# Performance work log

Measured on AMD Instinct MI355X. Metric: run time of the kernel, lower is better.

Reference implementation:

```python
import jax, jax.numpy as jnp
import numpy as np

TOP_K = 2
NORM_TOPK_PROB = True


def setup_inputs() -> dict:
    key = jax.random.key(0)
    k1, k2, k3, k4 = jax.random.split(key, 4)
    B, S, H = 1, 1024, 2048
    E, I = 16, 768
    hidden_states = jax.random.normal(k1, (B, S, H), dtype=jnp.float32)
    # 0.02 init scale keeps router logits / activations in a realistic range
    gate_w = jax.random.normal(k2, (E, H), dtype=jnp.float32) * 0.02
    w1 = jax.random.normal(k3, (E, 2 * I, H), dtype=jnp.float32) * 0.02  # [gate; up] stacked
    w2 = jax.random.normal(k4, (E, H, I), dtype=jnp.float32) * 0.02
    return {"hidden_states": hidden_states, "gate_w": gate_w, "w1": w1, "w2": w2}


def reference(hidden_states, gate_w, w1, w2):
    B, S, H = hidden_states.shape
    E = gate_w.shape[0]
    I = w2.shape[2]
    x = hidden_states.reshape(-1, H)  # [T, H]

    # Router
    router_logits = x @ gate_w.T  # [T, E]
    probs = jax.nn.softmax(router_logits.astype(jnp.float32), axis=-1)
    topk_w, topk_ids = jax.lax.top_k(probs, TOP_K)  # [T, K]
    if NORM_TOPK_PROB:
        topk_w = topk_w / jnp.sum(topk_w, axis=-1, keepdims=True)
    topk_w = topk_w.astype(x.dtype)

    # combine[t, e] = sum_k topk_w[t, k] * 1[topk_ids[t, k] == e]
    combine = jnp.sum(jax.nn.one_hot(topk_ids, E, dtype=x.dtype) * topk_w[..., None], axis=1)  # [T, E]

    def expert(w1_e, w2_e):
        h = x @ w1_e.T                      # [T, 2I]
        act = jax.nn.silu(h[:, :I]) * h[:, I:]  # fused SiLU-and-mul
        return act @ w2_e.T                 # [T, H]

    y_all = jax.vmap(expert)(w1, w2)        # [E, T, H]
    out = jnp.einsum('te,eth->th', combine, y_all)  # weighted scatter-sum over experts
    return out, router_logits
```

## Files before the change

### kernel.cpp

```cpp
#include <hip/hip_runtime.h>
#include <hip/hip_bf16.h>


#define T_TOK 1024
#define HDIM  2048
#define NEXP  16
#define IDIM  768
#define CAP   192

typedef __attribute__((ext_vector_type(8))) short  short8_t;
typedef __attribute__((ext_vector_type(4))) float  f32x4_t;

static __device__ __forceinline__ unsigned short f2bf(float f) {
  unsigned u = __float_as_uint(f);
  u += 0x7FFFu + ((u >> 16) & 1u);
  return (unsigned short)(u >> 16);
}
static __device__ __forceinline__ short f2bf_t(float f) {
  return (short)(__float_as_uint(f) >> 16);
}
static __device__ __forceinline__ float bf2f(unsigned short h) {
  return __uint_as_float(((unsigned)h) << 16);
}
static __device__ __forceinline__ void cvt_store4(unsigned short* dst, float4 v) {
  ushort4 u;
  u.x = f2bf(v.x); u.y = f2bf(v.y); u.z = f2bf(v.z); u.w = f2bf(v.w);
  *(ushort4*)dst = u;
}
static __device__ __forceinline__ short8_t pack_bf16(float4 lo, float4 hi) {
  short8_t r;
  r[0] = f2bf_t(lo.x); r[1] = f2bf_t(lo.y); r[2] = f2bf_t(lo.z); r[3] = f2bf_t(lo.w);
  r[4] = f2bf_t(hi.x); r[5] = f2bf_t(hi.y); r[6] = f2bf_t(hi.z); r[7] = f2bf_t(hi.w);
  return r;
}
static __device__ __forceinline__ void gl2lds16(const void* g, void* l) {
  __builtin_amdgcn_global_load_lds(
      (const __attribute__((address_space(1))) unsigned int*)g,
      (__attribute__((address_space(3))) unsigned int*)l, 16, 0, 0);
}

__global__ __launch_bounds__(256) void cvt_x(
    const float* __restrict__ x, unsigned short* __restrict__ xb) {
  int i = blockIdx.x * 256 + threadIdx.x;
  float4 v = ((const float4*)x)[i];
  cvt_store4(xb + (size_t)i * 4, v);
}

__global__ __launch_bounds__(256) void moe_router(
    const float* __restrict__ x, const float* __restrict__ gw,
    float* __restrict__ logits_out, int* __restrict__ cnt,
    int* __restrict__ tok, float* __restrict__ wl) {
  const int t = blockIdx.x;
  const int tid = threadIdx.x;
  const int lane = tid & 63, wid = tid >> 6;
  const float4* xv = (const float4*)(x + (size_t)t * HDIM);
  float4 v0 = xv[tid * 2], v1 = xv[tid * 2 + 1];
  float acc[NEXP];
#pragma unroll
  for (int e = 0; e < NEXP; ++e) {
    const float4* gv = (const float4*)(gw + (size_t)e * HDIM);
    float4 g0 = gv[tid * 2], g1 = gv[tid * 2 + 1];
    acc[e] = v0.x * g0.x + v0.y * g0.y + v0.z * g0.z + v0.w * g0.w +
             v1.x * g1.x + v1.y * g1.y + v1.z * g1.z + v1.w * g1.w;
  }
#pragma unroll
  for (int e = 0; e < NEXP; ++e)
#pragma unroll
    for (int off = 32; off; off >>= 1) acc[e] += __shfl_xor(acc[e], off, 64);
  __shared__ float red[4][NEXP];
  if (lane == 0)
#pragma unroll
    for (int e = 0; e < NEXP; ++e) red[wid][e] = acc[e];
  __syncthreads();
  if (tid < NEXP) {
    float s = red[0][tid] + red[1][tid] + red[2][tid] + red[3][tid];
    logits_out[(size_t)t * NEXP + tid] = s;
    red[0][tid] = s;
  }
  __syncthreads();
  if (tid == 0) {
    int e1 = -1, e2 = -1;
    float l1 = -1e30f, l2 = -1e30f;
#pragma unroll
    for (int e = 0; e < NEXP; ++e) {
      float v = red[0][e];
      if (v > l1)      { l2 = l1; e2 = e1; l1 = v; e1 = e; }
      else if (v > l2) { l2 = v;  e2 = e; }
    }
    float wa = 1.f / (1.f + __expf(l2 - l1));
    float wb = 1.f - wa;
    int p1 = atomicAdd(&cnt[e1], 1);
    if (p1 < CAP) { tok[e1 * CAP + p1] = t; wl[e1 * CAP + p1] = wa; }
    int p2 = atomicAdd(&cnt[e2], 1);
    if (p2 < CAP) { tok[e2 * CAP + p2] = t; wl[e2 * CAP + p2] = wb; }
  }
}

__global__ __launch_bounds__(256) void moe_stage_a(
    const unsigned short* __restrict__ xb, const float* __restrict__ w1,
    const int* __restrict__ cnt, const int* __restrict__ tok,
    unsigned short* __restrict__ h_ws) {
  int bx = blockIdx.x;
  const int ks = bx & 1;
  const int mt = (bx >> 1) & 1;
  const int nt = (bx >> 2) % 12;
  const int e  = (bx >> 2) / 12;
  int ne = cnt[e]; if (ne > CAP) ne = CAP;
  if (mt * 128 >= ne) return;

  __shared__ unsigned short As[128 * 32];
  __shared__ float          Bs[128 * 32];
  __shared__ int toksL[128];
  const int tid = threadIdx.x;
  if (tid < 128) {
    int idx = mt * 128 + tid;
    toksL[tid] = tok[e * CAP + (idx < ne ? idx : ne - 1)];
  }
  __syncthreads();

  const int w = tid >> 6, lane = tid & 63;
  const int k0 = ks * 1024;

  const unsigned short* aG[2];
  unsigned short* aL[2];
#pragma unroll
  for (int jj = 0; jj < 2; ++jj) {
    int j = w * 2 + jj;
    int row = 16 * j + (lane >> 2);
    aG[jj] = xb + (size_t)toksL[row] * HDIM + k0 + (lane & 3) * 8;
    aL[jj] = As + j * 512;
  }
  const float* bG[4];
  float* bL[4];
#pragma unroll
  for (int jj = 0; jj < 4; ++jj) {
    int j = w * 4 + jj;
    int nrow = 8 * j + (lane >> 3);
    int d = ((lane & 7) - (lane >> 3)) & 7;
    bG[jj] = w1 + ((size_t)e * (2 * IDIM) + nt * 128 + nrow) * HDIM + k0 + d * 4;
    bL[jj] = Bs + j * 256;
  }

  const int wr = w >> 1, wc = w & 1;
  const int quad = lane >> 4, lr = lane & 15;
  f32x4_t acc[4][4] = {};

  for (int kk = 0; kk < 1024; kk += 32) {
#pragma unroll
    for (int jj = 0; jj < 2; ++jj) gl2lds16(aG[jj] + kk, aL[jj]);
#pragma unroll
    for (int jj = 0; jj < 4; ++jj) gl2lds16(bG[jj] + kk, bL[jj]);
    __syncthreads();

    short8_t a[4], b[4];
#pragma unroll
    for (int mf = 0; mf < 4; ++mf) {
      int row = wr * 64 + mf * 16 + lr;
      a[mf] = *(const short8_t*)&As[row * 32 + quad * 8];
    }
#pragma unroll
    for (int nf = 0; nf < 4; ++nf) {
      int r = wc * 64 + nf * 16 + lr;
      int p0 = (2 * quad + r) & 7, p1 = (2 * quad + 1 + r) & 7;
      float4 f0 = *(const float4*)&Bs[r * 32 + p0 * 4];
      float4 f1 = *(const float4*)&Bs[r * 32 + p1 * 4];
      b[nf] = pack_bf16(f0, f1);
    }
#pragma unroll
    for (int mf = 0; mf < 4; ++mf)
#pragma unroll
      for (int nf = 0; nf < 4; ++nf)
        acc[mf][nf] = __builtin_amdgcn_mfma_f32_16x16x32_bf16(
            a[mf], b[nf], acc[mf][nf], 0, 0, 0);
    __syncthreads();
  }

  unsigned short* hp = h_ws + ((size_t)ks * NEXP + e) * CAP * (2 * IDIM);
#pragma unroll
  for (int mf = 0; mf < 4; ++mf) {
#pragma unroll
    for (int rr = 0; rr < 4; ++rr) {
      int mg = mt * 128 + wr * 64 + mf * 16 + quad * 4 + rr;
      if (mg < CAP) {
#pragma unroll
        for (int nf = 0; nf < 4; ++nf) {
          int ng = nt * 128 + wc * 64 + nf * 16 + lr;
          hp[(size_t)mg * (2 * IDIM) + ng] = f2bf(acc[mf][nf][rr]);
        }
      }
    }
  }
}

__global__ __launch_bounds__(256) void moe_merge(
    const unsigned short* __restrict__ h_ws, unsigned short* __restrict__ act) {
  const size_t part = (size_t)NEXP * CAP * (2 * IDIM);
  int c = blockIdx.x * 256 + threadIdx.x;
  int row = c / (IDIM / 4);
  int c4  = c % (IDIM / 4);
  size_t gb = (size_t)row * (2 * IDIM) + c4 * 4;
  ushort4 g0 = *(const ushort4*)(h_ws + gb);
  ushort4 g1 = *(const ushort4*)(h_ws + part + gb);
  ushort4 u0 = *(const ushort4*)(h_ws + gb + IDIM);
  ushort4 u1 = *(const ushort4*)(h_ws + part + gb + IDIM);
  float g, u; ushort4 o;
  g = bf2f(g0.x) + bf2f(g1.x); u = bf2f(u0.x) + bf2f(u1.x);
  o.x = f2bf(g / (1.f + __expf(-g)) * u);
  g = bf2f(g0.y) + bf2f(g1.y); u = bf2f(u0.y) + bf2f(u1.y);
  o.y = f2bf(g / (1.f + __expf(-g)) * u);
  g = bf2f(g0.z) + bf2f(g1.z); u = bf2f(u0.z) + bf2f(u1.z);
  o.z = f2bf(g / (1.f + __expf(-g)) * u);
  g = bf2f(g0.w) + bf2f(g1.w); u = bf2f(u0.w) + bf2f(u1.w);
  o.w = f2bf(g / (1.f + __expf(-g)) * u);
  *(ushort4*)(act + (size_t)row * IDIM + c4 * 4) = o;
}

__global__ __launch_bounds__(256) void moe_stage_b(
    const unsigned short* __restrict__ act, const float* __restrict__ w2,
    const int* __restrict__ cnt, const int* __restrict__ tok,
    const float* __restrict__ wl, float* __restrict__ out) {
  int bx = blockIdx.x;
  const int ks = bx & 1;
  const int mt = (bx >> 1) & 1;
  const int nt = (bx >> 2) & 15;
  const int e  = bx >> 6;
  int ne = cnt[e]; if (ne > CAP) ne = CAP;
  if (mt * 128 >= ne) return;

  __shared__ unsigned short As[128 * 32];
  __shared__ float          Bs[128 * 32];
  __shared__ int   toksL[128];
  __shared__ float wtsL[128];
  const int tid = threadIdx.x;
  if (tid < 128) {
    int idx = mt * 128 + tid;
    bool v = idx < ne;
    toksL[tid] = tok[e * CAP + (v ? idx : ne - 1)];
    wtsL[tid]  = v ? wl[e * CAP + idx] : 0.f;
  }
  __syncthreads();

  const int w = tid >> 6, lane = tid & 63;
  const int k0 = ks * 384;

  const unsigned short* aG[2];
  unsigned short* aL[2];
#pragma unroll
  for (int jj = 0; jj < 2; ++jj) {
    int j = w * 2 + jj;
    int slot = mt * 128 + 16 * j + (lane >> 2);
    if (slot >= CAP) slot = CAP - 1;
    aG[jj] = act + ((size_t)e * CAP + slot) * IDIM + k0 + (lane & 3) * 8;
    aL[jj] = As + j * 512;
  }
  const float* bG[4];
  float* bL[4];
#pragma unroll
  for (int jj = 0; jj < 4; ++jj) {
    int j = w * 4 + jj;
    int nrow = 8 * j + (lane >> 3);
    int d = ((lane & 7) - (lane >> 3)) & 7;
    bG[jj] = w2 + ((size_t)e * HDIM + nt * 128 + nrow) * IDIM + k0 + d * 4;
    bL[jj] = Bs + j * 256;
  }

  const int wr = w >> 1, wc = w & 1;
  const int quad = lane >> 4, lr = lane & 15;
  f32x4_t acc[4][4] = {};

  for (int kk = 0; kk < 384; kk += 32) {
#pragma unroll
    for (int jj = 0; jj < 2; ++jj) gl2lds16(aG[jj] + kk, aL[jj]);
#pragma unroll
    for (int jj = 0; jj < 4; ++jj) gl2lds16(bG[jj] + kk, bL[jj]);
    __syncthreads();

    short8_t a[4], b[4];
#pragma unroll
    for (int mf = 0; mf < 4; ++mf) {
      int row = wr * 64 + mf * 16 + lr;
      a[mf] = *(const short8_t*)&As[row * 32 + quad * 8];
    }
#pragma unroll
    for (int nf = 0; nf < 4; ++nf) {
      int r = wc * 64 + nf * 16 + lr;
      int p0 = (2 * quad + r) & 7, p1 = (2 * quad + 1 + r) & 7;
      float4 f0 = *(const float4*)&Bs[r * 32 + p0 * 4];
      float4 f1 = *(const float4*)&Bs[r * 32 + p1 * 4];
      b[nf] = pack_bf16(f0, f1);
    }
#pragma unroll
    for (int mf = 0; mf < 4; ++mf)
#pragma unroll
      for (int nf = 0; nf < 4; ++nf)
        acc[mf][nf] = __builtin_amdgcn_mfma_f32_16x16x32_bf16(
            a[mf], b[nf], acc[mf][nf], 0, 0, 0);
    __syncthreads();
  }

#pragma unroll
  for (int mf = 0; mf < 4; ++mf) {
#pragma unroll
    for (int rr = 0; rr < 4; ++rr) {
      int sl = wr * 64 + mf * 16 + quad * 4 + rr;
      if (mt * 128 + sl < ne) {
        float wgt = wtsL[sl];
        int   t   = toksL[sl];
#pragma unroll
        for (int nf = 0; nf < 4; ++nf) {
          int ng = nt * 128 + wc * 64 + nf * 16 + lr;
          atomicAdd(&out[(size_t)t * HDIM + ng], acc[mf][nf][rr] * wgt);
        }
      }
    }
  }
}

extern "C" void kernel_launch(void* const* d_in, const int* in_sizes, int n_in,
                              void* d_out, int out_size, void* d_ws,
                              size_t ws_size, hipStream_t stream) {
  (void)in_sizes; (void)n_in; (void)out_size; (void)ws_size;
  const float* x  = (const float*)d_in[0];
  const float* gw = (const float*)d_in[1];
  const float* w1 = (const float*)d_in[2];
  const float* w2 = (const float*)d_in[3];
  float* out    = (float*)d_out;
  float* logits = out + (size_t)T_TOK * HDIM;

  char* ws = (char*)d_ws;
  int*   cnt = (int*)ws;
  int*   tok = (int*)(ws + 256);
  float* wl  = (float*)(ws + 256 + NEXP * CAP * 4);
  unsigned short* xb  = (unsigned short*)(ws + 24832);
  unsigned short* act = xb;
  unsigned short* h_ws =
      (unsigned short*)(ws + 24832 + (size_t)NEXP * CAP * IDIM * 2);

  hipMemsetAsync(cnt, 0, 256, stream);
  hipMemsetAsync(d_out, 0, (size_t)T_TOK * HDIM * sizeof(float), stream);

  cvt_x      <<<T_TOK * HDIM / 4 / 256, 256, 0, stream>>>(x, xb);
  moe_router <<<T_TOK, 256, 0, stream>>>(x, gw, logits, cnt, tok, wl);
  moe_stage_a<<<NEXP * 12 * 2 * 2, 256, 0, stream>>>(xb, w1, cnt, tok, h_ws);
  moe_merge  <<<NEXP * CAP * IDIM / 4 / 256, 256, 0, stream>>>(h_ws, act);
  moe_stage_b<<<NEXP * 16 * 2 * 2, 256, 0, stream>>>(act, w2, cnt, tok, wl, out);
}
```

Before: 469.0 us.

## Retile expert GEMMs to full-capacity M=192 by N=64 tiles

Both expert GEMM stages change from 128x128 tiles split into two M tiles to a single 192-row tile covering the whole expert capacity, with a 64-wide N tile and each wave owning 48 rows. Each fp32 weight tile is now loaded from global memory once per expert instead of once per M tile. The per-row capacity guard in stage A's store is dropped since 192 equals CAP. The trade-off is that experts with fewer tokens always compute all 192 rows, and the activation tiles are re-read across twice as many N tiles.

```diff
diff --git a/kernel.cpp b/kernel.cpp
--- a/kernel.cpp
+++ b/kernel.cpp
@@ -102,72 +102,66 @@
     unsigned short* __restrict__ h_ws) {
   int bx = blockIdx.x;
   const int ks = bx & 1;
-  const int mt = (bx >> 1) & 1;
-  const int nt = (bx >> 2) % 12;
-  const int e  = (bx >> 2) / 12;
+  const int nt = (bx >> 1) % 24;
+  const int e  = (bx >> 1) / 24;
   int ne = cnt[e]; if (ne > CAP) ne = CAP;
-  if (mt * 128 >= ne) return;
-
-  __shared__ unsigned short As[128 * 32];
-  __shared__ float          Bs[128 * 32];
-  __shared__ int toksL[128];
+
+  __shared__ unsigned short As[192 * 32];
+  __shared__ float          Bs[64 * 32];
+  __shared__ int toksL[192];
   const int tid = threadIdx.x;
-  if (tid < 128) {
-    int idx = mt * 128 + tid;
-    toksL[tid] = tok[e * CAP + (idx < ne ? idx : ne - 1)];
-  }
+  if (tid < 192) toksL[tid] = tok[e * CAP + (tid < ne ? tid : ne - 1)];
   __syncthreads();
 
   const int w = tid >> 6, lane = tid & 63;
   const int k0 = ks * 1024;
 
-  const unsigned short* aG[2];
-  unsigned short* aL[2];
-#pragma unroll
-  for (int jj = 0; jj < 2; ++jj) {
-    int j = w * 2 + jj;
+  const unsigned short* aG[3];
+  unsigned short* aL[3];
+#pragma unroll
+  for (int jj = 0; jj < 3; ++jj) {
+    int j = w * 3 + jj;
     int row = 16 * j + (lane >> 2);
     aG[jj] = xb + (size_t)toksL[row] * HDIM + k0 + (lane & 3) * 8;
     aL[jj] = As + j * 512;
   }
-  const float* bG[4];
-  float* bL[4];
-#pragma unroll
-  for (int jj = 0; jj < 4; ++jj) {
-    int j = w * 4 + jj;
+  const float* bG[2];
+  float* bL[2];
+#pragma unroll
+  for (int jj = 0; jj < 2; ++jj) {
+    int j = w * 2 + jj;
     int nrow = 8 * j + (lane >> 3);
     int d = ((lane & 7) - (lane >> 3)) & 7;
-    bG[jj] = w1 + ((size_t)e * (2 * IDIM) + nt * 128 + nrow) * HDIM + k0 + d * 4;
+    bG[jj] = w1 + ((size_t)e * (2 * IDIM) + nt * 64 + nrow) * HDIM + k0 + d * 4;
     bL[jj] = Bs + j * 256;
   }
 
-  const int wr = w >> 1, wc = w & 1;
   const int quad = lane >> 4, lr = lane & 15;
-  f32x4_t acc[4][4] = {};
+  f32x4_t acc[3][4] = {};
 
   for (int kk = 0; kk < 1024; kk += 32) {
 #pragma unroll
-    for (int jj = 0; jj < 2; ++jj) gl2lds16(aG[jj] + kk, aL[jj]);
-#pragma unroll
-    for (int jj = 0; jj < 4; ++jj) gl2lds16(bG[jj] + kk, bL[jj]);
+    for (int jj = 0; jj < 3; ++jj) gl2lds16(aG[jj] + kk, aL[jj]);
+#pragma unroll
+    for (int jj = 0; jj < 2; ++jj) gl2lds16(bG[jj] + kk, bL[jj]);
     __syncthreads();
 
-    short8_t a[4], b[4];
-#pragma unroll
-    for (int mf = 0; mf < 4; ++mf) {
-      int row = wr * 64 + mf * 16 + lr;
+    short8_t a[3], b[4];
+#pragma unroll
+    for (int mf = 0; mf < 3; ++mf) {
+      int row = w * 48 + mf * 16 + lr;
       a[mf] = *(const short8_t*)&As[row * 32 + quad * 8];
     }
 #pragma unroll
     for (int nf = 0; nf < 4; ++nf) {
-      int r = wc * 64 + nf * 16 + lr;
+      int r = nf * 16 + lr;
       int p0 = (2 * quad + r) & 7, p1 = (2 * quad + 1 + r) & 7;
       float4 f0 = *(const float4*)&Bs[r * 32 + p0 * 4];
       float4 f1 = *(const float4*)&Bs[r * 32 + p1 * 4];
       b[nf] = pack_bf16(f0, f1);
     }
 #pragma unroll
-    for (int mf = 0; mf < 4; ++mf)
+    for (int mf = 0; mf < 3; ++mf)
 #pragma unroll
       for (int nf = 0; nf < 4; ++nf)
         acc[mf][nf] = __builtin_amdgcn_mfma_f32_16x16x32_bf16(
@@ -177,16 +171,14 @@
 
   unsigned short* hp = h_ws + ((size_t)ks * NEXP + e) * CAP * (2 * IDIM);
 #pragma unroll
-  for (int mf = 0; mf < 4; ++mf) {
+  for (int mf = 0; mf < 3; ++mf) {
 #pragma unroll
     for (int rr = 0; rr < 4; ++rr) {
-      int mg = mt * 128 + wr * 64 + mf * 16 + quad * 4 + rr;
-      if (mg < CAP) {
-#pragma unroll
-        for (int nf = 0; nf < 4; ++nf) {
-          int ng = nt * 128 + wc * 64 + nf * 16 + lr;
-          hp[(size_t)mg * (2 * IDIM) + ng] = f2bf(acc[mf][nf][rr]);
-        }
+      int mg = w * 48 + mf * 16 + quad * 4 + rr;
+#pragma unroll
+      for (int nf = 0; nf < 4; ++nf) {
+        int ng = nt * 64 + nf * 16 + lr;
+        hp[(size_t)mg * (2 * IDIM) + ng] = f2bf(acc[mf][nf][rr]);
       }
     }
   }
@@ -221,76 +213,71 @@
     const float* __restrict__ wl, float* __restrict__ out) {
   int bx = blockIdx.x;
   const int ks = bx & 1;
-  const int mt = (bx >> 1) & 1;
-  const int nt = (bx >> 2) & 15;
+  const int nt = (bx >> 1) & 31;
   const int e  = bx >> 6;
   int ne = cnt[e]; if (ne > CAP) ne = CAP;
-  if (mt * 128 >= ne) return;
-
-  __shared__ unsigned short As[128 * 32];
-  __shared__ float          Bs[128 * 32];
-  __shared__ int   toksL[128];
-  __shared__ float wtsL[128];
+
+  __shared__ unsigned short As[192 * 32];
+  __shared__ float          Bs[64 * 32];
+  __shared__ int   toksL[192];
+  __shared__ float wtsL[192];
   const int tid = threadIdx.x;
-  if (tid < 128) {
-    int idx = mt * 128 + tid;
-    bool v = idx < ne;
-    toksL[tid] = tok[e * CAP + (v ? idx : ne - 1)];
-    wtsL[tid]  = v ? wl[e * CAP + idx] : 0.f;
+  if (tid < 192) {
+    bool v = tid < ne;
+    toksL[tid] = tok[e * CAP + (v ? tid : ne - 1)];
+    wtsL[tid]  = v ? wl[e * CAP + tid] : 0.f;
   }
   __syncthreads();
 
   const int w = tid >> 6, lane = tid & 63;
   const int k0 = ks * 384;
 
-  const unsigned short* aG[2];
-  unsigned short* aL[2];
+  const unsigned short* aG[3];
+  unsigned short* aL[3];
+#pragma unroll
+  for (int jj = 0; jj < 3; ++jj) {
+    int j = w * 3 + jj;
+    int slot = 16 * j + (lane >> 2);
+    aG[jj] = act + ((size_t)e * CAP + slot) * IDIM + k0 + (lane & 3) * 8;
+    aL[jj] = As + j * 512;
+  }
+  const float* bG[2];
+  float* bL[2];
 #pragma unroll
   for (int jj = 0; jj < 2; ++jj) {
     int j = w * 2 + jj;
-    int slot = mt * 128 + 16 * j + (lane >> 2);
-    if (slot >= CAP) slot = CAP - 1;
-    aG[jj] = act + ((size_t)e * CAP + slot) * IDIM + k0 + (lane & 3) * 8;
-    aL[jj] = As + j * 512;
-  }
-  const float* bG[4];
-  float* bL[4];
-#pragma unroll
-  for (int jj = 0; jj < 4; ++jj) {
-    int j = w * 4 + jj;
     int nrow = 8 * j + (lane >> 3);
     int d = ((lane & 7) - (lane >> 3)) & 7;
-    bG[jj] = w2 + ((size_t)e * HDIM + nt * 128 + nrow) * IDIM + k0 + d * 4;
+    bG[jj] = w2 + ((size_t)e * HDIM + nt * 64 + nrow) * IDIM + k0 + d * 4;
     bL[jj] = Bs + j * 256;
   }
 
-  const int wr = w >> 1, wc = w & 1;
   const int quad = lane >> 4, lr = lane & 15;
-  f32x4_t acc[4][4] = {};
+  f32x4_t acc[3][4] = {};
 
   for (int kk = 0; kk < 384; kk += 32) {
 #pragma unroll
-    for (int jj = 0; jj < 2; ++jj) gl2lds16(aG[jj] + kk, aL[jj]);
-#pragma unroll
-    for (int jj = 0; jj < 4; ++jj) gl2lds16(bG[jj] + kk, bL[jj]);
+    for (int jj = 0; jj < 3; ++jj) gl2lds16(aG[jj] + kk, aL[jj]);
+#pragma unroll
+    for (int jj = 0; jj < 2; ++jj) gl2lds16(bG[jj] + kk, bL[jj]);
     __syncthreads();
 
-    short8_t a[4], b[4];
-#pragma unroll
-    for (int mf = 0; mf < 4; ++mf) {
-      int row = wr * 64 + mf * 16 + lr;
+    short8_t a[3], b[4];
+#pragma unroll
+    for (int mf = 0; mf < 3; ++mf) {
+      int row = w * 48 + mf * 16 + lr;
       a[mf] = *(const short8_t*)&As[row * 32 + quad * 8];
     }
 #pragma unroll
     for (int nf = 0; nf < 4; ++nf) {
-      int r = wc * 64 + nf * 16 + lr;
+      int r = nf * 16 + lr;
       int p0 = (2 * quad + r) & 7, p1 = (2 * quad + 1 + r) & 7;
       float4 f0 = *(const float4*)&Bs[r * 32 + p0 * 4];
       float4 f1 = *(const float4*)&Bs[r * 32 + p1 * 4];
       b[nf] = pack_bf16(f0, f1);
     }
 #pragma unroll
-    for (int mf = 0; mf < 4; ++mf)
+    for (int mf = 0; mf < 3; ++mf)
 #pragma unroll
       for (int nf = 0; nf < 4; ++nf)
         acc[mf][nf] = __builtin_amdgcn_mfma_f32_16x16x32_bf16(
@@ -299,16 +286,16 @@
   }
 
 #pragma unroll
-  for (int mf = 0; mf < 4; ++mf) {
+  for (int mf = 0; mf < 3; ++mf) {
 #pragma unroll
     for (int rr = 0; rr < 4; ++rr) {
-      int sl = wr * 64 + mf * 16 + quad * 4 + rr;
-      if (mt * 128 + sl < ne) {
+      int sl = w * 48 + mf * 16 + quad * 4 + rr;
+      if (sl < ne) {
         float wgt = wtsL[sl];
         int   t   = toksL[sl];
 #pragma unroll
         for (int nf = 0; nf < 4; ++nf) {
-          int ng = nt * 128 + wc * 64 + nf * 16 + lr;
+          int ng = nt * 64 + nf * 16 + lr;
           atomicAdd(&out[(size_t)t * HDIM + ng], acc[mf][nf][rr] * wgt);
         }
       }
@@ -341,7 +328,7 @@
 
   cvt_x      <<<T_TOK * HDIM / 4 / 256, 256, 0, stream>>>(x, xb);
   moe_router <<<T_TOK, 256, 0, stream>>>(x, gw, logits, cnt, tok, wl);
-  moe_stage_a<<<NEXP * 12 * 2 * 2, 256, 0, stream>>>(xb, w1, cnt, tok, h_ws);
+  moe_stage_a<<<NEXP * 24 * 2, 256, 0, stream>>>(xb, w1, cnt, tok, h_ws);
   moe_merge  <<<NEXP * CAP * IDIM / 4 / 256, 256, 0, stream>>>(h_ws, act);
-  moe_stage_b<<<NEXP * 16 * 2 * 2, 256, 0, stream>>>(act, w2, cnt, tok, wl, out);
-}
+  moe_stage_b<<<NEXP * 32 * 2, 256, 0, stream>>>(act, w2, cnt, tok, wl, out);
+}
```

New measurement: 444.1 us. 5.3% less time.
